# Kernel optimization log

Hardware: AMD Instinct MI355X
Metric: run time of the kernel (lower is better)

## Reference

```python
import jax, jax.numpy as jnp
import numpy as np

N = 100000      # nodes
E = 3200000     # edges (avg degree 32)
IN = 128        # in_channels
H = 32          # hidden dim
OUT = 64        # out_channels
L = 31          # number of SGConv layers


def setup_inputs() -> dict:
    key = jax.random.key(0)
    ks = jax.random.split(key, 10)
    x = jax.random.normal(ks[0], (N, IN), dtype=jnp.float32)
    edge_index = jax.random.randint(ks[1], (2, E), 0, N, dtype=jnp.int32)
    s = 0.05
    W1 = jax.random.normal(ks[2], (H, IN), dtype=jnp.float32) * s
    b1 = jnp.zeros((H,), dtype=jnp.float32)
    Wc = jax.random.normal(ks[3], (L, H, H), dtype=jnp.float32) * s
    bc = jnp.zeros((L, H), dtype=jnp.float32)
    W32 = jax.random.normal(ks[4], (OUT, 32 * H), dtype=jnp.float32) * s
    b32 = jnp.zeros((OUT,), dtype=jnp.float32)
    return {"x": x, "edge_index": edge_index, "W1": W1, "b1": b1,
            "Wc": Wc, "bc": bc, "W32": W32, "b32": b32}


def mynorm(t):
    # min/max over feature axis (dim=1 of [N, C]; last axis in general)
    mn = jnp.min(t, axis=-1, keepdims=True)
    mx = jnp.max(t, axis=-1, keepdims=True)
    return 2.0 * (t - mn) / (mx - mn + 1e-8) - 1.0


def reference(x, edge_index, W1, b1, Wc, bc, W32, b32):
    n = x.shape[0]
    loops = jnp.arange(n, dtype=edge_index.dtype)
    row = jnp.concatenate([edge_index[0], loops])  # source
    col = jnp.concatenate([edge_index[1], loops])  # target
    # symmetric GCN normalization (PyG gcn_norm, add_self_loops=True)
    deg = jax.ops.segment_sum(jnp.ones_like(row, dtype=x.dtype), col, num_segments=n)
    dis = jnp.where(deg > 0, jax.lax.rsqrt(deg), 0.0)
    nrm = (dis[row] * dis[col])[:, None]  # [E+N, 1]

    def prop(h):
        # out[col] += norm * h[row]
        return jax.ops.segment_sum(h[row] * nrm, col, num_segments=n)

    x0 = mynorm(jax.nn.relu(x @ W1.T + b1))  # [N, 32]

    def step(h, p):
        W, b = p
        y = prop(h) @ W.T + b  # SGConv K=1: propagate then linear
        return y, y

    _, ys = jax.lax.scan(step, x0, (Wc, bc))  # [31, N, 32]
    xs = jnp.concatenate([x0[None], ys], axis=0)  # [32, N, 32]
    m = mynorm(xs)
    # xx1 = x1; xxk = mynorm(xk) - mynorm(x_{k-2}); original uses raw x16 at slot 16
    feats = [x0, xs[1]]
    for k in range(2, 32):
        feats.append(xs[k] if k == 16 else m[k] - m[k - 2])
    cat = jnp.concatenate(feats, axis=1)  # [N, 1024]
    return cat @ W32.T + b32  # [N, 64]
```

## Files before the change

kernel.cpp:

```cpp
#include <hip/hip_runtime.h>
#include <hip/hip_fp16.h>

#define NN 100000
#define NE 3200000
#define NB8 12500

__global__ __launch_bounds__(256) void k_deg(const int* __restrict__ col, int* __restrict__ deg) {
    int e = blockIdx.x * 256 + threadIdx.x;
    if (e < NE) atomicAdd(&deg[col[e]], 1);
}

__global__ __launch_bounds__(256) void k_bsum(const int* __restrict__ deg, int* __restrict__ bsum) {
    __shared__ int s[256];
    int t = threadIdx.x, i = blockIdx.x * 256 + t;
    s[t] = (i < NN) ? deg[i] : 0;
    __syncthreads();
    for (int st = 128; st > 0; st >>= 1) {
        if (t < st) s[t] += s[t + st];
        __syncthreads();
    }
    if (t == 0) bsum[blockIdx.x] = s[0];
}

__global__ __launch_bounds__(512) void k_scanb(int* __restrict__ bsum, int nb) {
    __shared__ int s[512];
    int t = threadIdx.x;
    s[t] = (t < nb) ? bsum[t] : 0;
    __syncthreads();
    for (int off = 1; off < 512; off <<= 1) {
        int v = (t >= off) ? s[t - off] : 0;
        __syncthreads();
        s[t] += v;
        __syncthreads();
    }
    if (t < nb) bsum[t] = (t == 0) ? 0 : s[t - 1];
}

__global__ __launch_bounds__(256) void k_colptr(const int* __restrict__ deg, const int* __restrict__ bsum,
                                                int* __restrict__ colptr) {
    __shared__ int s[256];
    int t = threadIdx.x, i = blockIdx.x * 256 + t;
    int v = (i < NN) ? deg[i] : 0;
    s[t] = v;
    __syncthreads();
    for (int off = 1; off < 256; off <<= 1) {
        int u = (t >= off) ? s[t - off] : 0;
        __syncthreads();
        s[t] += u;
        __syncthreads();
    }
    if (i <= NN) colptr[i] = bsum[blockIdx.x] + s[t] - v;
}

__global__ __launch_bounds__(256) void k_dis(int* __restrict__ degdis) {
    int i = blockIdx.x * 256 + threadIdx.x;
    if (i < NN) {
        int d = degdis[i];
        ((float*)degdis)[i] = 1.0f / sqrtf((float)(d + 1));
    }
}

__global__ __launch_bounds__(256) void k_scatter(const int* __restrict__ ei, const int* __restrict__ colptr,
                                                 int* __restrict__ cursor, int* __restrict__ csr_row, int p) {
    int e = blockIdx.x * 256 + threadIdx.x;
    if (e < NE) {
        int c = ei[NE + e];
        int lo = p * NB8;
        if (c >= lo && c < lo + NB8) {
            int r = ei[e];
            int pos = colptr[c] + atomicAdd(&cursor[c], 1);
            csr_row[pos] = r;
        }
    }
}

__global__ __launch_bounds__(256) void k_x0(const float* __restrict__ x, const float* __restrict__ W1,
                                            const float* __restrict__ b1, const float* __restrict__ W32,
                                            const float* __restrict__ b32, const float* __restrict__ dis,
                                            __half* __restrict__ h0, __half* __restrict__ ring0,
                                            float* __restrict__ out, float* __restrict__ Mhat,
                                            float* __restrict__ SCar) {
    __shared__ float sW1[32 * 128];
    __shared__ float sW32[64 * 32];
    __shared__ float sb1[32], sb32[64];
    int t = threadIdx.x;
    if (blockIdx.x == 0 && t == 0) SCar[0] = 1.0f;
    for (int i = t; i < 4096; i += 256) sW1[i] = W1[i];
    for (int i = t; i < 2048; i += 256) sW32[i] = W32[(i >> 5) * 1024 + (i & 31)];
    if (t < 32) sb1[t] = b1[t];
    if (t < 64) sb32[t] = b32[t];
    __syncthreads();
    int node = blockIdx.x * 256 + t;
    if (node >= NN) return;

    float acc[32];
#pragma unroll
    for (int c = 0; c < 32; c++) acc[c] = sb1[c];
    const float4* xr4 = (const float4*)(x + (long)node * 128);
    for (int q = 0; q < 32; q++) {
        float4 xv = xr4[q];
#pragma unroll
        for (int c = 0; c < 32; c++) {
            acc[c] += xv.x * sW1[c * 128 + q * 4] + xv.y * sW1[c * 128 + q * 4 + 1] +
                      xv.z * sW1[c * 128 + q * 4 + 2] + xv.w * sW1[c * 128 + q * 4 + 3];
        }
    }
    float mn = 1e30f, mx = -1e30f;
#pragma unroll
    for (int c = 0; c < 32; c++) {
        acc[c] = fmaxf(acc[c], 0.f);
        mn = fminf(mn, acc[c]);
        mx = fmaxf(mx, acc[c]);
    }
    float inv = 2.f / (mx - mn + 1e-8f);
#pragma unroll
    for (int c = 0; c < 32; c++) acc[c] = inv * (acc[c] - mn) - 1.f;
    float sc = dis[node];
    __half2* hr = (__half2*)(h0 + (long)node * 32);
#pragma unroll
    for (int q = 0; q < 16; q++) hr[q] = __floats2half2_rn(sc * acc[2 * q], sc * acc[2 * q + 1]);
    if (t == 0 && (blockIdx.x & 15) == 0) atomicMax((int*)&Mhat[0], __float_as_int(sc));
    float mn2 = 1e30f, mx2 = -1e30f;
#pragma unroll
    for (int c = 0; c < 32; c++) {
        mn2 = fminf(mn2, acc[c]);
        mx2 = fmaxf(mx2, acc[c]);
    }
    float inv2 = 2.f / (mx2 - mn2 + 1e-8f);
    __half2* rr = (__half2*)(ring0 + (long)node * 32);
#pragma unroll
    for (int q = 0; q < 16; q++)
        rr[q] = __floats2half2_rn(inv2 * (acc[2 * q] - mn2) - 1.f, inv2 * (acc[2 * q + 1] - mn2) - 1.f);
    float* orow = out + (long)node * 64;
    for (int o = 0; o < 64; o++) {
        float a = sb32[o];
#pragma unroll
        for (int j = 0; j < 32; j++) a += sW32[o * 32 + j] * acc[j];
        orow[o] = a;
    }
}

__global__ __launch_bounds__(256, 3) void k_layer(const __half* __restrict__ hin, __half* __restrict__ hout,
                                                  __half* __restrict__ ring, const float* __restrict__ dis,
                                                  const int* __restrict__ colptr, const int* __restrict__ csr_row,
                                                  const float* __restrict__ Wck, const float* __restrict__ bck,
                                                  const float* __restrict__ W32k, float* __restrict__ out,
                                                  float* __restrict__ Mhat, float* __restrict__ SCar, int k,
                                                  int rawfeat) {
    __shared__ float sWc[32 * 33];
    __shared__ float sW[64 * 33];
    __shared__ float sbc[32];
    int t = threadIdx.x;
    float SCin = SCar[k - 1];
    float SCk = SCin * fmaxf(Mhat[k - 1], 1e-30f);
    if (t == 0) SCar[k] = SCk;
    float invSCk = 1.0f / SCk;
    for (int i = t; i < 1024; i += 256) sWc[(i >> 5) * 33 + (i & 31)] = Wck[i];
    for (int i = t; i < 2048; i += 256) sW[(i >> 5) * 33 + (i & 31)] = W32k[(i >> 5) * 1024 + (i & 31)];
    if (t < 32) sbc[t] = bck[t];
    __syncthreads();

    int wave = t >> 6, lane = t & 63;
    int sub = lane >> 3, q = lane & 7;
    int node = blockIdx.x * 32 + wave * 8 + sub;
    int sl = sub * 8;

    const uint2* __restrict__ h2 = (const uint2*)hin;
    int e0 = colptr[node], e1 = colptr[node + 1];
    float di = dis[node];

    float a0, a1, a2, a3, b0 = 0.f, b1 = 0.f, b2 = 0.f, b3 = 0.f;
    {
        uint2 u = h2[(long)node * 8 + q];
        float2 lo = __half22float2(*(__half2*)&u.x);
        float2 hi = __half22float2(*(__half2*)&u.y);
        a0 = lo.x; a1 = lo.y; a2 = hi.x; a3 = hi.y;
    }
    int base = e0;
    while (base + 8 <= e1) {
        int r = csr_row[base + q];
#pragma unroll
        for (int j = 0; j < 8; j += 2) {
            int r0 = __shfl(r, sl + j, 64);
            int r1 = __shfl(r, sl + j + 1, 64);
            uint2 u0 = h2[(long)r0 * 8 + q];
            uint2 u1 = h2[(long)r1 * 8 + q];
            float2 lo0 = __half22float2(*(__half2*)&u0.x), hi0 = __half22float2(*(__half2*)&u0.y);
            float2 lo1 = __half22float2(*(__half2*)&u1.x), hi1 = __half22float2(*(__half2*)&u1.y);
            a0 += lo0.x; a1 += lo0.y; a2 += hi0.x; a3 += hi0.y;
            b0 += lo1.x; b1 += lo1.y; b2 += hi1.x; b3 += hi1.y;
        }
        base += 8;
    }
    int rem = e1 - base;
    if (rem > 0) {
        int r = (q < rem) ? csr_row[base + q] : 0;
        for (int j = 0; j < rem; j++) {
            int rj = __shfl(r, sl + j, 64);
            uint2 u = h2[(long)rj * 8 + q];
            float2 lo = __half22float2(*(__half2*)&u.x), hi = __half22float2(*(__half2*)&u.y);
            a0 += lo.x; a1 += lo.y; a2 += hi.x; a3 += hi.y;
        }
    }
    float g0 = di * (a0 + b0), g1 = di * (a1 + b1), g2 = di * (a2 + b2), g3 = di * (a3 + b3);

    const float* wr0 = &sWc[(4 * q + 0) * 33];
    const float* wr1 = &sWc[(4 * q + 1) * 33];
    const float* wr2 = &sWc[(4 * q + 2) * 33];
    const float* wr3 = &sWc[(4 * q + 3) * 33];
    float y0 = 0.f, y1 = 0.f, y2 = 0.f, y3 = 0.f;
#pragma unroll
    for (int s = 0; s < 8; s++) {
        float t0 = __shfl(g0, sl + s, 64);
        float t1 = __shfl(g1, sl + s, 64);
        float t2 = __shfl(g2, sl + s, 64);
        float t3 = __shfl(g3, sl + s, 64);
        int jb = 4 * s;
        y0 += wr0[jb] * t0 + wr0[jb + 1] * t1 + wr0[jb + 2] * t2 + wr0[jb + 3] * t3;
        y1 += wr1[jb] * t0 + wr1[jb + 1] * t1 + wr1[jb + 2] * t2 + wr1[jb + 3] * t3;
        y2 += wr2[jb] * t0 + wr2[jb + 1] * t1 + wr2[jb + 2] * t2 + wr2[jb + 3] * t3;
        y3 += wr3[jb] * t0 + wr3[jb + 1] * t1 + wr3[jb + 2] * t2 + wr3[jb + 3] * t3;
    }
    y0 = SCin * y0 + sbc[4 * q + 0];
    y1 = SCin * y1 + sbc[4 * q + 1];
    y2 = SCin * y2 + sbc[4 * q + 2];
    y3 = SCin * y3 + sbc[4 * q + 3];

    {
        __half2 p0 = __floats2half2_rn(di * y0 * invSCk, di * y1 * invSCk);
        __half2 p1 = __floats2half2_rn(di * y2 * invSCk, di * y3 * invSCk);
        uint2 pw;
        pw.x = *(unsigned int*)&p0;
        pw.y = *(unsigned int*)&p1;
        ((uint2*)hout)[(long)node * 8 + q] = pw;
    }

    float mn = fminf(fminf(y0, y1), fminf(y2, y3));
    float mx = fmaxf(fmaxf(y0, y1), fmaxf(y2, y3));
#pragma unroll
    for (int m = 1; m < 8; m <<= 1) {
        mn = fminf(mn, __shfl_xor(mn, m, 64));
        mx = fmaxf(mx, __shfl_xor(mx, m, 64));
    }
    float inv = 2.f / (mx - mn + 1e-8f);
    float mv0 = inv * (y0 - mn) - 1.f, mv1 = inv * (y1 - mn) - 1.f;
    float mv2 = inv * (y2 - mn) - 1.f, mv3 = inv * (y3 - mn) - 1.f;

    if ((blockIdx.x & 15) == 0 && q == 0) {
        float rowmax = fmaxf(fabsf(mn), fabsf(mx));
        atomicMax((int*)&Mhat[k], __float_as_int(di * rowmax * invSCk));
    }

    float f0, f1, f2, f3;
    if (rawfeat) {
        f0 = y0; f1 = y1; f2 = y2; f3 = y3;
    } else {
        uint2 rv = ((const uint2*)ring)[(long)node * 8 + q];
        float2 rlo = __half22float2(*(__half2*)&rv.x);
        float2 rhi = __half22float2(*(__half2*)&rv.y);
        f0 = mv0 - rlo.x; f1 = mv1 - rlo.y; f2 = mv2 - rhi.x; f3 = mv3 - rhi.y;
    }
    {
        __half2 p0 = __floats2half2_rn(mv0, mv1);
        __half2 p1 = __floats2half2_rn(mv2, mv3);
        uint2 pw;
        pw.x = *(unsigned int*)&p0;
        pw.y = *(unsigned int*)&p1;
        ((uint2*)ring)[(long)node * 8 + q] = pw;
    }

    float o0 = 0.f, o1 = 0.f, o2 = 0.f, o3 = 0.f, o4 = 0.f, o5 = 0.f, o6 = 0.f, o7 = 0.f;
#pragma unroll
    for (int s = 0; s < 8; s++) {
        float t0 = __shfl(f0, sl + s, 64);
        float t1 = __shfl(f1, sl + s, 64);
        float t2 = __shfl(f2, sl + s, 64);
        float t3 = __shfl(f3, sl + s, 64);
        int jb = 4 * s;
        const float* w = &sW[(8 * q) * 33 + jb];
        o0 += w[0] * t0 + w[1] * t1 + w[2] * t2 + w[3] * t3; w += 33;
        o1 += w[0] * t0 + w[1] * t1 + w[2] * t2 + w[3] * t3; w += 33;
        o2 += w[0] * t0 + w[1] * t1 + w[2] * t2 + w[3] * t3; w += 33;
        o3 += w[0] * t0 + w[1] * t1 + w[2] * t2 + w[3] * t3; w += 33;
        o4 += w[0] * t0 + w[1] * t1 + w[2] * t2 + w[3] * t3; w += 33;
        o5 += w[0] * t0 + w[1] * t1 + w[2] * t2 + w[3] * t3; w += 33;
        o6 += w[0] * t0 + w[1] * t1 + w[2] * t2 + w[3] * t3; w += 33;
        o7 += w[0] * t0 + w[1] * t1 + w[2] * t2 + w[3] * t3;
    }
    float4* op = (float4*)(out + (long)node * 64 + 8 * q);
    float4 v0 = op[0], v1 = op[1];
    v0.x += o0; v0.y += o1; v0.z += o2; v0.w += o3;
    v1.x += o4; v1.y += o5; v1.z += o6; v1.w += o7;
    op[0] = v0;
    op[1] = v1;
}

extern "C" void kernel_launch(void* const* d_in, const int* in_sizes, int n_in, void* d_out, int out_size,
                              void* d_ws, size_t ws_size, hipStream_t stream) {
    const float* x = (const float*)d_in[0];
    const int* ei = (const int*)d_in[1];
    const float* W1 = (const float*)d_in[2];
    const float* b1 = (const float*)d_in[3];
    const float* Wc = (const float*)d_in[4];
    const float* bc = (const float*)d_in[5];
    const float* W32 = (const float*)d_in[6];
    const float* b32 = (const float*)d_in[7];
    float* out = (float*)d_out;

    int* deg = (int*)d_ws;
    int* cursor = deg + NN;
    float* Mhat = (float*)(cursor + NN);
    float* SCar = Mhat + 64;
    int* colptr = (int*)(SCar + 64);
    int* bsum = colptr + 100004;
    int* csr_row = bsum + 1024;
    __half* h0 = (__half*)(csr_row + NE);
    __half* h1 = h0 + (long)NN * 32;
    __half* ring = h1 + (long)NN * 32;
    float* dis = (float*)deg;

    hipMemsetAsync(deg, 0, (2 * NN + 128) * sizeof(int), stream);
    k_deg<<<(NE + 255) / 256, 256, 0, stream>>>(ei + NE, deg);
    int NB = (NN + 255) / 256;
    k_bsum<<<NB, 256, 0, stream>>>(deg, bsum);
    k_scanb<<<1, 512, 0, stream>>>(bsum, NB);
    k_colptr<<<NB, 256, 0, stream>>>(deg, bsum, colptr);
    k_dis<<<(NN + 255) / 256, 256, 0, stream>>>(deg);
    for (int p = 0; p < 8; p++)
        k_scatter<<<(NE + 255) / 256, 256, 0, stream>>>(ei, colptr, cursor, csr_row, p);
    k_x0<<<NB, 256, 0, stream>>>(x, W1, b1, W32, b32, dis, h0, ring, out, Mhat, SCar);

    for (int k = 1; k <= 31; k++) {
        const __half* hin = (k & 1) ? h0 : h1;
        __half* hout = (k & 1) ? h1 : h0;
        __half* ringk = ring + (long)(k & 1) * NN * 32;
        int raw = (k == 1 || k == 16) ? 1 : 0;
        k_layer<<<3125, 256, 0, stream>>>(hin, hout, ringk, dis, colptr, csr_row, Wc + (k - 1) * 1024,
                                          bc + (k - 1) * 32, W32 + 32 * k, out, Mhat, SCar, k, raw);
    }
}
```

Before: 2.703 ms.

## Accumulate output in fp16 with nontemporal accesses and halve scatter passes

The running output accumulator moves from fp32 to fp16, and a final kernel converts it back to fp32. This halves the read-modify-write traffic on the output in each of the 31 layer kernels. Loads and stores of csr_row, ring, hout and the output now use nontemporal hints, and the CSR scatter runs in 4 partition passes instead of 8. Summing 32 terms into an fp16 accumulator adds rounding error that could break accuracy tolerance, and wider scatter partitions raise atomic contention.

```diff
diff --git a/kernel.cpp b/kernel.cpp
--- a/kernel.cpp
+++ b/kernel.cpp
@@ -3,7 +3,19 @@
 
 #define NN 100000
 #define NE 3200000
-#define NB8 12500
+#define NB8 25000
+
+typedef unsigned int uint2v __attribute__((ext_vector_type(2)));
+typedef unsigned int uint4v __attribute__((ext_vector_type(4)));
+
+static __device__ __forceinline__ float2 h2f(unsigned int u) {
+    __half2 h = *(__half2*)&u;
+    return __half22float2(h);
+}
+static __device__ __forceinline__ unsigned int f2h(float a, float b) {
+    __half2 h = __floats2half2_rn(a, b);
+    return *(unsigned int*)&h;
+}
 
 __global__ __launch_bounds__(256) void k_deg(const int* __restrict__ col, int* __restrict__ deg) {
     int e = blockIdx.x * 256 + threadIdx.x;
@@ -78,7 +90,7 @@
                                             const float* __restrict__ b1, const float* __restrict__ W32,
                                             const float* __restrict__ b32, const float* __restrict__ dis,
                                             __half* __restrict__ h0, __half* __restrict__ ring0,
-                                            float* __restrict__ out, float* __restrict__ Mhat,
+                                            __half* __restrict__ out_h, float* __restrict__ Mhat,
                                             float* __restrict__ SCar) {
     __shared__ float sW1[32 * 128];
     __shared__ float sW32[64 * 32];
@@ -131,12 +143,12 @@
 #pragma unroll
     for (int q = 0; q < 16; q++)
         rr[q] = __floats2half2_rn(inv2 * (acc[2 * q] - mn2) - 1.f, inv2 * (acc[2 * q + 1] - mn2) - 1.f);
-    float* orow = out + (long)node * 64;
+    __half* orow = out_h + (long)node * 64;
     for (int o = 0; o < 64; o++) {
         float a = sb32[o];
 #pragma unroll
         for (int j = 0; j < 32; j++) a += sW32[o * 32 + j] * acc[j];
-        orow[o] = a;
+        orow[o] = __float2half(a);
     }
 }
 
@@ -144,7 +156,7 @@
                                                   __half* __restrict__ ring, const float* __restrict__ dis,
                                                   const int* __restrict__ colptr, const int* __restrict__ csr_row,
                                                   const float* __restrict__ Wck, const float* __restrict__ bck,
-                                                  const float* __restrict__ W32k, float* __restrict__ out,
+                                                  const float* __restrict__ W32k, __half* __restrict__ out_h,
                                                   float* __restrict__ Mhat, float* __restrict__ SCar, int k,
                                                   int rawfeat) {
     __shared__ float sWc[32 * 33];
@@ -172,21 +184,20 @@
     float a0, a1, a2, a3, b0 = 0.f, b1 = 0.f, b2 = 0.f, b3 = 0.f;
     {
         uint2 u = h2[(long)node * 8 + q];
-        float2 lo = __half22float2(*(__half2*)&u.x);
-        float2 hi = __half22float2(*(__half2*)&u.y);
+        float2 lo = h2f(u.x), hi = h2f(u.y);
         a0 = lo.x; a1 = lo.y; a2 = hi.x; a3 = hi.y;
     }
     int base = e0;
     while (base + 8 <= e1) {
-        int r = csr_row[base + q];
+        int r = __builtin_nontemporal_load(csr_row + base + q);
 #pragma unroll
         for (int j = 0; j < 8; j += 2) {
             int r0 = __shfl(r, sl + j, 64);
             int r1 = __shfl(r, sl + j + 1, 64);
             uint2 u0 = h2[(long)r0 * 8 + q];
             uint2 u1 = h2[(long)r1 * 8 + q];
-            float2 lo0 = __half22float2(*(__half2*)&u0.x), hi0 = __half22float2(*(__half2*)&u0.y);
-            float2 lo1 = __half22float2(*(__half2*)&u1.x), hi1 = __half22float2(*(__half2*)&u1.y);
+            float2 lo0 = h2f(u0.x), hi0 = h2f(u0.y);
+            float2 lo1 = h2f(u1.x), hi1 = h2f(u1.y);
             a0 += lo0.x; a1 += lo0.y; a2 += hi0.x; a3 += hi0.y;
             b0 += lo1.x; b1 += lo1.y; b2 += hi1.x; b3 += hi1.y;
         }
@@ -198,7 +209,7 @@
         for (int j = 0; j < rem; j++) {
             int rj = __shfl(r, sl + j, 64);
             uint2 u = h2[(long)rj * 8 + q];
-            float2 lo = __half22float2(*(__half2*)&u.x), hi = __half22float2(*(__half2*)&u.y);
+            float2 lo = h2f(u.x), hi = h2f(u.y);
             a0 += lo.x; a1 += lo.y; a2 += hi.x; a3 += hi.y;
         }
     }
@@ -227,12 +238,10 @@
     y3 = SCin * y3 + sbc[4 * q + 3];
 
     {
-        __half2 p0 = __floats2half2_rn(di * y0 * invSCk, di * y1 * invSCk);
-        __half2 p1 = __floats2half2_rn(di * y2 * invSCk, di * y3 * invSCk);
-        uint2 pw;
-        pw.x = *(unsigned int*)&p0;
-        pw.y = *(unsigned int*)&p1;
-        ((uint2*)hout)[(long)node * 8 + q] = pw;
+        uint2v pw;
+        pw.x = f2h(di * y0 * invSCk, di * y1 * invSCk);
+        pw.y = f2h(di * y2 * invSCk, di * y3 * invSCk);
+        __builtin_nontemporal_store(pw, (uint2v*)((uint2*)hout + (long)node * 8 + q));
     }
 
     float mn = fminf(fminf(y0, y1), fminf(y2, y3));
@@ -255,18 +264,16 @@
     if (rawfeat) {
         f0 = y0; f1 = y1; f2 = y2; f3 = y3;
     } else {
-        uint2 rv = ((const uint2*)ring)[(long)node * 8 + q];
-        float2 rlo = __half22float2(*(__half2*)&rv.x);
-        float2 rhi = __half22float2(*(__half2*)&rv.y);
+        uint2v rv = __builtin_nontemporal_load((const uint2v*)((const uint2*)ring + (long)node * 8 + q));
+        unsigned int rx = rv.x, ry = rv.y;
+        float2 rlo = h2f(rx), rhi = h2f(ry);
         f0 = mv0 - rlo.x; f1 = mv1 - rlo.y; f2 = mv2 - rhi.x; f3 = mv3 - rhi.y;
     }
     {
-        __half2 p0 = __floats2half2_rn(mv0, mv1);
-        __half2 p1 = __floats2half2_rn(mv2, mv3);
-        uint2 pw;
-        pw.x = *(unsigned int*)&p0;
-        pw.y = *(unsigned int*)&p1;
-        ((uint2*)ring)[(long)node * 8 + q] = pw;
+        uint2v pw;
+        pw.x = f2h(mv0, mv1);
+        pw.y = f2h(mv2, mv3);
+        __builtin_nontemporal_store(pw, (uint2v*)((uint2*)ring + (long)node * 8 + q));
     }
 
     float o0 = 0.f, o1 = 0.f, o2 = 0.f, o3 = 0.f, o4 = 0.f, o5 = 0.f, o6 = 0.f, o7 = 0.f;
@@ -287,12 +294,27 @@
         o6 += w[0] * t0 + w[1] * t1 + w[2] * t2 + w[3] * t3; w += 33;
         o7 += w[0] * t0 + w[1] * t1 + w[2] * t2 + w[3] * t3;
     }
-    float4* op = (float4*)(out + (long)node * 64 + 8 * q);
-    float4 v0 = op[0], v1 = op[1];
-    v0.x += o0; v0.y += o1; v0.z += o2; v0.w += o3;
-    v1.x += o4; v1.y += o5; v1.z += o6; v1.w += o7;
-    op[0] = v0;
-    op[1] = v1;
+    uint4v* op = (uint4v*)(out_h + (long)node * 64 + 8 * q);
+    uint4v ov = __builtin_nontemporal_load(op);
+    unsigned int w0 = ov.x, w1 = ov.y, w2 = ov.z, w3 = ov.w;
+    float2 f01 = h2f(w0), f23 = h2f(w1), f45 = h2f(w2), f67 = h2f(w3);
+    uint4v nv;
+    nv.x = f2h(f01.x + o0, f01.y + o1);
+    nv.y = f2h(f23.x + o2, f23.y + o3);
+    nv.z = f2h(f45.x + o4, f45.y + o5);
+    nv.w = f2h(f67.x + o6, f67.y + o7);
+    __builtin_nontemporal_store(nv, op);
+}
+
+__global__ __launch_bounds__(256) void k_fin(const __half* __restrict__ out_h, float* __restrict__ out) {
+    int i = blockIdx.x * 256 + threadIdx.x;
+    if (i >= NN * 8) return;
+    uint4v v = __builtin_nontemporal_load((const uint4v*)(out_h + (long)i * 8));
+    unsigned int w0 = v.x, w1 = v.y, w2 = v.z, w3 = v.w;
+    float2 f01 = h2f(w0), f23 = h2f(w1), f45 = h2f(w2), f67 = h2f(w3);
+    float4* o = (float4*)(out + (long)i * 8);
+    o[0] = make_float4(f01.x, f01.y, f23.x, f23.y);
+    o[1] = make_float4(f45.x, f45.y, f67.x, f67.y);
 }
 
 extern "C" void kernel_launch(void* const* d_in, const int* in_sizes, int n_in, void* d_out, int out_size,
@@ -317,6 +339,7 @@
     __half* h0 = (__half*)(csr_row + NE);
     __half* h1 = h0 + (long)NN * 32;
     __half* ring = h1 + (long)NN * 32;
+    __half* out_h = ring + (long)2 * NN * 32;
     float* dis = (float*)deg;
 
     hipMemsetAsync(deg, 0, (2 * NN + 128) * sizeof(int), stream);
@@ -326,9 +349,9 @@
     k_scanb<<<1, 512, 0, stream>>>(bsum, NB);
     k_colptr<<<NB, 256, 0, stream>>>(deg, bsum, colptr);
     k_dis<<<(NN + 255) / 256, 256, 0, stream>>>(deg);
-    for (int p = 0; p < 8; p++)
+    for (int p = 0; p < 4; p++)
         k_scatter<<<(NE + 255) / 256, 256, 0, stream>>>(ei, colptr, cursor, csr_row, p);
-    k_x0<<<NB, 256, 0, stream>>>(x, W1, b1, W32, b32, dis, h0, ring, out, Mhat, SCar);
+    k_x0<<<NB, 256, 0, stream>>>(x, W1, b1, W32, b32, dis, h0, ring, out_h, Mhat, SCar);
 
     for (int k = 1; k <= 31; k++) {
         const __half* hin = (k & 1) ? h0 : h1;
@@ -336,6 +359,7 @@
         __half* ringk = ring + (long)(k & 1) * NN * 32;
         int raw = (k == 1 || k == 16) ? 1 : 0;
         k_layer<<<3125, 256, 0, stream>>>(hin, hout, ringk, dis, colptr, csr_row, Wc + (k - 1) * 1024,
-                                          bc + (k - 1) * 32, W32 + 32 * k, out, Mhat, SCar, k, raw);
-    }
-}
+                                          bc + (k - 1) * 32, W32 + 32 * k, out_h, Mhat, SCar, k, raw);
+    }
+    k_fin<<<(NN * 8 + 255) / 256, 256, 0, stream>>>(out_h, out);
+}
```

Measured after the change: 2.936 ms. +8.6%, slower.

## Fuse all 31 propagation layers into one persistent cooperative kernel

Applied to the files above, without the earlier changes.

Replaces 31 separate layer launches with a single cooperative kernel of 625 blocks. Each block handles 5 node groups and keeps the output accumulators in registers across all layers, with grid-wide syncs between layers. This removes per-layer launch overhead and the repeated read-modify-write of the 64-wide output per layer. The cost is grid-sync latency, lower occupancy from the register-resident accumulators, and a dependence on cooperative launch being supported. The old per-layer path stays as a fallback.

```diff
diff --git a/kernel.cpp b/kernel.cpp
--- a/kernel.cpp
+++ b/kernel.cpp
@@ -1,9 +1,14 @@
 #include <hip/hip_runtime.h>
 #include <hip/hip_fp16.h>
+#include <hip/hip_cooperative_groups.h>
+
+namespace cg = cooperative_groups;
 
 #define NN 100000
 #define NE 3200000
 #define NB8 12500
+#define NBLK 625
+#define MAXG 5
 
 __global__ __launch_bounds__(256) void k_deg(const int* __restrict__ col, int* __restrict__ deg) {
     int e = blockIdx.x * 256 + threadIdx.x;
@@ -295,6 +300,193 @@
     op[1] = v1;
 }
 
+__global__ __launch_bounds__(256, 3) void k_layers(__half* __restrict__ h0buf, __half* __restrict__ h1buf,
+                                                   __half* __restrict__ ring2, const float* __restrict__ dis,
+                                                   const int* __restrict__ colptr, const int* __restrict__ csr_row,
+                                                   const float* __restrict__ Wc, const float* __restrict__ bc,
+                                                   const float* __restrict__ W32, float* __restrict__ out,
+                                                   float* __restrict__ Mhat) {
+    cg::grid_group gg = cg::this_grid();
+    __shared__ float sWc[32 * 33];
+    __shared__ float sW[64 * 33];
+    __shared__ float sbc[32];
+    __shared__ float sM;
+    int t = threadIdx.x;
+    int wave = t >> 6, lane = t & 63;
+    int sub = lane >> 3, q = lane & 7;
+    int sl = sub * 8;
+
+    float oa[MAXG][8];
+#pragma unroll
+    for (int i = 0; i < MAXG; i++) {
+        int node = (blockIdx.x + i * NBLK) * 32 + wave * 8 + sub;
+        const float4* op = (const float4*)(out + (long)node * 64 + 8 * q);
+        float4 v0 = op[0], v1 = op[1];
+        oa[i][0] = v0.x; oa[i][1] = v0.y; oa[i][2] = v0.z; oa[i][3] = v0.w;
+        oa[i][4] = v1.x; oa[i][5] = v1.y; oa[i][6] = v1.z; oa[i][7] = v1.w;
+    }
+
+    float SC = 1.0f;
+    for (int k = 1; k <= 31; k++) {
+        const __half* hin = (k & 1) ? h0buf : h1buf;
+        __half* hout = (k & 1) ? h1buf : h0buf;
+        __half* ring = ring2 + (long)(k & 1) * NN * 32;
+        int rawfeat = (k == 1 || k == 16) ? 1 : 0;
+        const float* Wck = Wc + (long)(k - 1) * 1024;
+        const float* bck = bc + (long)(k - 1) * 32;
+        const float* W32k = W32 + 32 * k;
+
+        if (t == 0) sM = __int_as_float(atomicMax((int*)&Mhat[k - 1], 0));
+        for (int i = t; i < 1024; i += 256) sWc[(i >> 5) * 33 + (i & 31)] = Wck[i];
+        for (int i = t; i < 2048; i += 256) sW[(i >> 5) * 33 + (i & 31)] = W32k[(i >> 5) * 1024 + (i & 31)];
+        if (t < 32) sbc[t] = bck[t];
+        __syncthreads();
+        float SCin = SC;
+        float SCk = SCin * fmaxf(sM, 1e-30f);
+        float invSCk = 1.0f / SCk;
+        const uint2* __restrict__ h2 = (const uint2*)hin;
+
+#pragma unroll
+        for (int i = 0; i < MAXG; i++) {
+            int grp = blockIdx.x + i * NBLK;
+            int node = grp * 32 + wave * 8 + sub;
+            int e0 = colptr[node], e1 = colptr[node + 1];
+            float di = dis[node];
+
+            float a0, a1, a2, a3, b0 = 0.f, b1 = 0.f, b2 = 0.f, b3 = 0.f;
+            {
+                uint2 u = h2[(long)node * 8 + q];
+                float2 lo = __half22float2(*(__half2*)&u.x);
+                float2 hi = __half22float2(*(__half2*)&u.y);
+                a0 = lo.x; a1 = lo.y; a2 = hi.x; a3 = hi.y;
+            }
+            int base = e0;
+            while (base + 8 <= e1) {
+                int r = csr_row[base + q];
+#pragma unroll
+                for (int j = 0; j < 8; j += 2) {
+                    int r0 = __shfl(r, sl + j, 64);
+                    int r1 = __shfl(r, sl + j + 1, 64);
+                    uint2 u0 = h2[(long)r0 * 8 + q];
+                    uint2 u1 = h2[(long)r1 * 8 + q];
+                    float2 lo0 = __half22float2(*(__half2*)&u0.x), hi0 = __half22float2(*(__half2*)&u0.y);
+                    float2 lo1 = __half22float2(*(__half2*)&u1.x), hi1 = __half22float2(*(__half2*)&u1.y);
+                    a0 += lo0.x; a1 += lo0.y; a2 += hi0.x; a3 += hi0.y;
+                    b0 += lo1.x; b1 += lo1.y; b2 += hi1.x; b3 += hi1.y;
+                }
+                base += 8;
+            }
+            int rem = e1 - base;
+            if (rem > 0) {
+                int r = (q < rem) ? csr_row[base + q] : 0;
+                for (int j = 0; j < rem; j++) {
+                    int rj = __shfl(r, sl + j, 64);
+                    uint2 u = h2[(long)rj * 8 + q];
+                    float2 lo = __half22float2(*(__half2*)&u.x), hi = __half22float2(*(__half2*)&u.y);
+                    a0 += lo.x; a1 += lo.y; a2 += hi.x; a3 += hi.y;
+                }
+            }
+            float g0 = di * (a0 + b0), g1 = di * (a1 + b1), g2 = di * (a2 + b2), g3 = di * (a3 + b3);
+
+            const float* wr0 = &sWc[(4 * q + 0) * 33];
+            const float* wr1 = &sWc[(4 * q + 1) * 33];
+            const float* wr2 = &sWc[(4 * q + 2) * 33];
+            const float* wr3 = &sWc[(4 * q + 3) * 33];
+            float y0 = 0.f, y1 = 0.f, y2 = 0.f, y3 = 0.f;
+#pragma unroll
+            for (int s = 0; s < 8; s++) {
+                float t0 = __shfl(g0, sl + s, 64);
+                float t1 = __shfl(g1, sl + s, 64);
+                float t2 = __shfl(g2, sl + s, 64);
+                float t3 = __shfl(g3, sl + s, 64);
+                int jb = 4 * s;
+                y0 += wr0[jb] * t0 + wr0[jb + 1] * t1 + wr0[jb + 2] * t2 + wr0[jb + 3] * t3;
+                y1 += wr1[jb] * t0 + wr1[jb + 1] * t1 + wr1[jb + 2] * t2 + wr1[jb + 3] * t3;
+                y2 += wr2[jb] * t0 + wr2[jb + 1] * t1 + wr2[jb + 2] * t2 + wr2[jb + 3] * t3;
+                y3 += wr3[jb] * t0 + wr3[jb + 1] * t1 + wr3[jb + 2] * t2 + wr3[jb + 3] * t3;
+            }
+            y0 = SCin * y0 + sbc[4 * q + 0];
+            y1 = SCin * y1 + sbc[4 * q + 1];
+            y2 = SCin * y2 + sbc[4 * q + 2];
+            y3 = SCin * y3 + sbc[4 * q + 3];
+
+            {
+                __half2 p0 = __floats2half2_rn(di * y0 * invSCk, di * y1 * invSCk);
+                __half2 p1 = __floats2half2_rn(di * y2 * invSCk, di * y3 * invSCk);
+                uint2 pw;
+                pw.x = *(unsigned int*)&p0;
+                pw.y = *(unsigned int*)&p1;
+                ((uint2*)hout)[(long)node * 8 + q] = pw;
+            }
+
+            float mn = fminf(fminf(y0, y1), fminf(y2, y3));
+            float mx = fmaxf(fmaxf(y0, y1), fmaxf(y2, y3));
+#pragma unroll
+            for (int m = 1; m < 8; m <<= 1) {
+                mn = fminf(mn, __shfl_xor(mn, m, 64));
+                mx = fmaxf(mx, __shfl_xor(mx, m, 64));
+            }
+            float inv = 2.f / (mx - mn + 1e-8f);
+            float mv0 = inv * (y0 - mn) - 1.f, mv1 = inv * (y1 - mn) - 1.f;
+            float mv2 = inv * (y2 - mn) - 1.f, mv3 = inv * (y3 - mn) - 1.f;
+
+            if ((grp & 15) == 0 && q == 0) {
+                float rowmax = fmaxf(fabsf(mn), fabsf(mx));
+                atomicMax((int*)&Mhat[k], __float_as_int(di * rowmax * invSCk));
+            }
+
+            float f0, f1, f2, f3;
+            if (rawfeat) {
+                f0 = y0; f1 = y1; f2 = y2; f3 = y3;
+            } else {
+                uint2 rv = ((const uint2*)ring)[(long)node * 8 + q];
+                float2 rlo = __half22float2(*(__half2*)&rv.x);
+                float2 rhi = __half22float2(*(__half2*)&rv.y);
+                f0 = mv0 - rlo.x; f1 = mv1 - rlo.y; f2 = mv2 - rhi.x; f3 = mv3 - rhi.y;
+            }
+            {
+                __half2 p0 = __floats2half2_rn(mv0, mv1);
+                __half2 p1 = __floats2half2_rn(mv2, mv3);
+                uint2 pw;
+                pw.x = *(unsigned int*)&p0;
+                pw.y = *(unsigned int*)&p1;
+                ((uint2*)ring)[(long)node * 8 + q] = pw;
+            }
+
+#pragma unroll
+            for (int s = 0; s < 8; s++) {
+                float t0 = __shfl(f0, sl + s, 64);
+                float t1 = __shfl(f1, sl + s, 64);
+                float t2 = __shfl(f2, sl + s, 64);
+                float t3 = __shfl(f3, sl + s, 64);
+                int jb = 4 * s;
+                const float* w = &sW[(8 * q) * 33 + jb];
+                oa[i][0] += w[0] * t0 + w[1] * t1 + w[2] * t2 + w[3] * t3; w += 33;
+                oa[i][1] += w[0] * t0 + w[1] * t1 + w[2] * t2 + w[3] * t3; w += 33;
+                oa[i][2] += w[0] * t0 + w[1] * t1 + w[2] * t2 + w[3] * t3; w += 33;
+                oa[i][3] += w[0] * t0 + w[1] * t1 + w[2] * t2 + w[3] * t3; w += 33;
+                oa[i][4] += w[0] * t0 + w[1] * t1 + w[2] * t2 + w[3] * t3; w += 33;
+                oa[i][5] += w[0] * t0 + w[1] * t1 + w[2] * t2 + w[3] * t3; w += 33;
+                oa[i][6] += w[0] * t0 + w[1] * t1 + w[2] * t2 + w[3] * t3; w += 33;
+                oa[i][7] += w[0] * t0 + w[1] * t1 + w[2] * t2 + w[3] * t3;
+            }
+        }
+
+        __threadfence_system();
+        gg.sync();
+        __threadfence_system();
+        SC = SCk;
+    }
+
+#pragma unroll
+    for (int i = 0; i < MAXG; i++) {
+        int node = (blockIdx.x + i * NBLK) * 32 + wave * 8 + sub;
+        float4* op = (float4*)(out + (long)node * 64 + 8 * q);
+        op[0] = make_float4(oa[i][0], oa[i][1], oa[i][2], oa[i][3]);
+        op[1] = make_float4(oa[i][4], oa[i][5], oa[i][6], oa[i][7]);
+    }
+}
+
 extern "C" void kernel_launch(void* const* d_in, const int* in_sizes, int n_in, void* d_out, int out_size,
                               void* d_ws, size_t ws_size, hipStream_t stream) {
     const float* x = (const float*)d_in[0];
@@ -330,12 +522,23 @@
         k_scatter<<<(NE + 255) / 256, 256, 0, stream>>>(ei, colptr, cursor, csr_row, p);
     k_x0<<<NB, 256, 0, stream>>>(x, W1, b1, W32, b32, dis, h0, ring, out, Mhat, SCar);
 
-    for (int k = 1; k <= 31; k++) {
-        const __half* hin = (k & 1) ? h0 : h1;
-        __half* hout = (k & 1) ? h1 : h0;
-        __half* ringk = ring + (long)(k & 1) * NN * 32;
-        int raw = (k == 1 || k == 16) ? 1 : 0;
-        k_layer<<<3125, 256, 0, stream>>>(hin, hout, ringk, dis, colptr, csr_row, Wc + (k - 1) * 1024,
-                                          bc + (k - 1) * 32, W32 + 32 * k, out, Mhat, SCar, k, raw);
-    }
-}
+    int nb = 0;
+    hipError_t qerr = hipOccupancyMaxActiveBlocksPerMultiprocessor(&nb, (const void*)k_layers, 256, 0);
+    bool coop_ok = false;
+    if (qerr == hipSuccess && nb >= 3) {
+        void* args[] = {(void*)&h0, (void*)&h1, (void*)&ring, (void*)&dis, (void*)&colptr,
+                        (void*)&csr_row, (void*)&Wc, (void*)&bc, (void*)&W32, (void*)&out, (void*)&Mhat};
+        hipError_t lerr = hipLaunchCooperativeKernel((void*)k_layers, dim3(NBLK), dim3(256), args, 0, stream);
+        coop_ok = (lerr == hipSuccess);
+    }
+    if (!coop_ok) {
+        for (int k = 1; k <= 31; k++) {
+            const __half* hin = (k & 1) ? h0 : h1;
+            __half* hout = (k & 1) ? h1 : h0;
+            __half* ringk = ring + (long)(k & 1) * NN * 32;
+            int raw = (k == 1 || k == 16) ? 1 : 0;
+            k_layer<<<3125, 256, 0, stream>>>(hin, hout, ringk, dis, colptr, csr_row, Wc + (k - 1) * 1024,
+                                              bc + (k - 1) * 32, W32 + 32 * k, out, Mhat, SCar, k, raw);
+        }
+    }
+}
```

Result: no change. 2.681 ms (-0.8%).
